# Optimization experiments

Measured on AMD Instinct MI355X. Metric: run time of the kernel, lower is better.

## Reference

```python
import jax, jax.numpy as jnp
import numpy as np

N = 100000   # nodes
E = 1600000  # edges (avg degree 16)
IN = 128     # in_size == out_size (required by layer stacking)
H = 4        # heads
D = 32       # per-head dim = out_size / heads
L = 3        # n_layers
NEG_SLOPE = 0.2  # DGL GATConv default leaky_relu slope


def setup_inputs() -> dict:
    key = jax.random.key(0)
    ks = jax.random.split(key, 7)
    h = jax.random.normal(ks[0], (N, IN), dtype=jnp.float32)
    src = jax.random.randint(ks[1], (E,), 0, N, dtype=jnp.int32)
    dst = jax.random.randint(ks[2], (E,), 0, N, dtype=jnp.int32)
    Ws = jax.random.normal(ks[3], (L, IN, H * D), dtype=jnp.float32) * 0.05
    attn_l = jax.random.normal(ks[4], (L, H, D), dtype=jnp.float32) * 0.05
    attn_r = jax.random.normal(ks[5], (L, H, D), dtype=jnp.float32) * 0.05
    bias = jnp.zeros((L, H, D), dtype=jnp.float32)
    return {"h": h, "src": src, "dst": dst, "Ws": Ws,
            "attn_l": attn_l, "attn_r": attn_r, "bias": bias}


def _gat_layer(h, src, dst, W, al, ar, b):
    # linear projection (no bias), reshape to heads
    ft = (h @ W).reshape(N, H, D)                       # [N,H,D]
    el = jnp.einsum('nhd,hd->nh', ft, al)               # [N,H]
    er = jnp.einsum('nhd,hd->nh', ft, ar)               # [N,H]
    # edge attention logits
    e = jax.nn.leaky_relu(el[src] + er[dst], NEG_SLOPE)  # [E,H]
    # segment softmax over incoming edges of each destination node
    m = jax.ops.segment_max(e, dst, num_segments=N)     # [N,H]
    m = jnp.where(jnp.isfinite(m), m, jnp.zeros_like(m))  # zero in-degree guard
    ee = jnp.exp(e - m[dst])                            # [E,H]
    den = jax.ops.segment_sum(ee, dst, num_segments=N)  # [N,H]
    a = ee / jnp.maximum(den[dst], 1e-9)                # [E,H]
    # weighted scatter-sum of source messages
    rst = jax.ops.segment_sum(ft[src] * a[:, :, None], dst, num_segments=N)  # [N,H,D]
    # residual (Identity: in_feats == H*D), bias, ELU activation
    rst = rst + h.reshape(N, H, D) + b
    return jax.nn.elu(rst), a


def reference(h, src, dst, Ws, attn_l, attn_r, bias):
    x = h
    a = None
    for i in range(L):
        out, a = _gat_layer(x, src, dst, Ws[i], attn_l[i], attn_r[i], bias[i])
        x = out.reshape(N, H * D)  # flatten(1)
    return x, a[:, :, None]  # ([N, H*D], [E, H, 1]) as DGL returns
```

## Files before the change

### kernel.cpp

```cpp
#include <hip/hip_runtime.h>
#include <hip/hip_bf16.h>
#include <math.h>

#define NN 100000
#define EE 1600000
#define IN_F 128
#define HH 4
#define DD 32
#define LL 3
#define NB_ 391
#define EPB 4096

typedef __bf16 bf16x8 __attribute__((ext_vector_type(8)));
typedef float f32x4 __attribute__((ext_vector_type(4)));

static __device__ __forceinline__ unsigned short f2bf(float x) {
    __hip_bfloat16 b = __float2bfloat16(x);
    return *reinterpret_cast<unsigned short*>(&b);
}

__global__ void wt_kernel(const float* __restrict__ Ws,
                          unsigned short* __restrict__ wt) {
    const int i = blockIdx.x * blockDim.x + threadIdx.x;
    if (i >= LL * IN_F * IN_F) return;
    const int l = i >> 14, r = i & 16383;
    const int n = r >> 7, k = r & 127;
    wt[i] = f2bf(Ws[(l << 14) + k * IN_F + n]);
}

template <bool F32A>
__global__ __launch_bounds__(256) void gemm_mfma_kernel(
    const void* __restrict__ a_src,
    const unsigned short* __restrict__ wt,
    const float* __restrict__ al,
    const float* __restrict__ ar,
    unsigned short* __restrict__ ft_bf,
    float* __restrict__ el,
    float* __restrict__ er) {
    const int wave = (blockIdx.x * blockDim.x + threadIdx.x) >> 6;
    const int lane = threadIdx.x & 63;
    const int base = wave * 16;
    if (base >= NN) return;
    const int c = lane & 15;
    const int quad = lane >> 4;

    const int arow = min(base + c, NN - 1);
    bf16x8 a[4];
    if (F32A) {
        const float4* xp = (const float4*)((const float*)a_src + (size_t)arow * IN_F);
#pragma unroll
        for (int kc = 0; kc < 4; ++kc) {
            const float4 lo = xp[(kc * 4 + quad) * 2];
            const float4 hi = xp[(kc * 4 + quad) * 2 + 1];
            union { unsigned short us[8]; bf16x8 v; } u;
            u.us[0] = f2bf(lo.x); u.us[1] = f2bf(lo.y);
            u.us[2] = f2bf(lo.z); u.us[3] = f2bf(lo.w);
            u.us[4] = f2bf(hi.x); u.us[5] = f2bf(hi.y);
            u.us[6] = f2bf(hi.z); u.us[7] = f2bf(hi.w);
            a[kc] = u.v;
        }
    } else {
        const bf16x8* ap = (const bf16x8*)((const unsigned short*)a_src + (size_t)arow * IN_F);
#pragma unroll
        for (int kc = 0; kc < 4; ++kc) a[kc] = ap[kc * 4 + quad];
    }

    f32x4 acc[8];
#pragma unroll
    for (int nt = 0; nt < 8; ++nt) {
        const bf16x8* bp = (const bf16x8*)(wt + (size_t)(nt * 16 + c) * IN_F);
        f32x4 d = {0.f, 0.f, 0.f, 0.f};
#pragma unroll
        for (int kc = 0; kc < 4; ++kc)
            d = __builtin_amdgcn_mfma_f32_16x16x32_bf16(a[kc], bp[kc * 4 + quad], d, 0, 0, 0);
        acc[nt] = d;
    }

#pragma unroll
    for (int r = 0; r < 4; ++r) {
        const int n = base + quad * 4 + r;
        if (n < NN) {
#pragma unroll
            for (int nt = 0; nt < 8; ++nt)
                ft_bf[(size_t)n * IN_F + nt * 16 + c] = f2bf(acc[nt][r]);
        }
    }

#pragma unroll
    for (int h = 0; h < 4; ++h) {
        float pl[4], pr[4];
#pragma unroll
        for (int r = 0; r < 4; ++r) {
            const float a0 = acc[2 * h][r], a1 = acc[2 * h + 1][r];
            pl[r] = a0 * al[h * 32 + c] + a1 * al[h * 32 + 16 + c];
            pr[r] = a0 * ar[h * 32 + c] + a1 * ar[h * 32 + 16 + c];
        }
#pragma unroll
        for (int off = 8; off >= 1; off >>= 1) {
#pragma unroll
            for (int r = 0; r < 4; ++r) {
                pl[r] += __shfl_xor(pl[r], off);
                pr[r] += __shfl_xor(pr[r], off);
            }
        }
        if (c == 0) {
#pragma unroll
            for (int r = 0; r < 4; ++r) {
                const int n = base + quad * 4 + r;
                if (n < NN) {
                    el[n * HH + h] = pl[r];
                    er[n * HH + h] = pr[r];
                }
            }
        }
    }
}


__global__ void bucket_hist_kernel(const int* __restrict__ dst,
                                   int* __restrict__ tot) {
    __shared__ int l[NB_];
    for (int b = threadIdx.x; b < NB_; b += 256) l[b] = 0;
    __syncthreads();
    const int e0 = blockIdx.x * EPB;
    const int e1 = min(e0 + EPB, EE);
    for (int e = e0 + threadIdx.x; e < e1; e += 256)
        atomicAdd(&l[dst[e] >> 8], 1);
    __syncthreads();
    for (int b = threadIdx.x; b < NB_; b += 256)
        if (l[b]) atomicAdd(&tot[b], l[b]);
}

__global__ void bucket_scan_kernel(const int* __restrict__ tot,
                                   int* __restrict__ base,
                                   int* __restrict__ cur) {
    __shared__ int tmp[512];
    const int tid = threadIdx.x;
    int v = (tid < NB_) ? tot[tid] : 0;
    tmp[tid] = v;
    __syncthreads();
    for (int off = 1; off < 512; off <<= 1) {
        int t = (tid >= off) ? tmp[tid - off] : 0;
        __syncthreads();
        if (tid >= off) tmp[tid] += t;
        __syncthreads();
    }
    if (tid < NB_) {
        const int excl = tmp[tid] - v;
        base[tid] = excl;
        cur[tid] = excl;
    }
    if (tid == 0) base[NB_] = EE;
}

__global__ void partition_kernel(const int* __restrict__ src,
                                 const int* __restrict__ dst,
                                 int* __restrict__ cur,
                                 int* __restrict__ bkt) {
    __shared__ int lcnt[NB_];
    __shared__ int lbase[NB_];
    const int tid = threadIdx.x;
    const int e0 = blockIdx.x * EPB;
    const int e1 = min(e0 + EPB, EE);
    for (int b = tid; b < NB_; b += 256) lcnt[b] = 0;
    __syncthreads();
    for (int e = e0 + tid; e < e1; e += 256)
        atomicAdd(&lcnt[dst[e] >> 8], 1);
    __syncthreads();
    for (int b = tid; b < NB_; b += 256) {
        const int c = lcnt[b];
        lbase[b] = c ? atomicAdd(&cur[b], c) : 0;
        lcnt[b] = 0;
    }
    __syncthreads();
    for (int e = e0 + tid; e < e1; e += 256) {
        const int d = dst[e];
        const int b = d >> 8;
        const int idx = atomicAdd(&lcnt[b], 1);
        bkt[lbase[b] + idx] = ((d & 255) << 17) | src[e];
    }
}

__global__ void bucket_sort_kernel(const int* __restrict__ bkt,
                                   const int* __restrict__ base,
                                   int* __restrict__ cnt,
                                   int* __restrict__ row_start,
                                   int* __restrict__ ssrc) {
    __shared__ int lcnt[256];
    __shared__ int loff[256];
    const int tid = threadIdx.x;
    const int b = blockIdx.x;
    const int s0 = base[b], s1 = base[b + 1];
    lcnt[tid] = 0;
    __syncthreads();
    for (int p = s0 + tid; p < s1; p += 256)
        atomicAdd(&lcnt[bkt[p] >> 17], 1);
    __syncthreads();
    const int v = lcnt[tid];
    loff[tid] = v;
    __syncthreads();
    for (int off = 1; off < 256; off <<= 1) {
        int t = (tid >= off) ? loff[tid - off] : 0;
        __syncthreads();
        if (tid >= off) loff[tid] += t;
        __syncthreads();
    }
    const int excl = loff[tid] - v;
    const int n = b * 256 + tid;
    if (n < NN) {
        cnt[n] = v;
        row_start[n] = s0 + excl;
    }
    __syncthreads();
    loff[tid] = excl;
    lcnt[tid] = 0;
    __syncthreads();
    for (int p = s0 + tid; p < s1; p += 256) {
        const int w = bkt[p];
        const int dl = w >> 17;
        const int idx = atomicAdd(&lcnt[dl], 1);
        ssrc[s0 + loff[dl] + idx] = w & 0x1FFFF;
    }
}

__global__ void aggregate_kernel(const uint4* __restrict__ ft4,
                                 const float* __restrict__ el,
                                 const float* __restrict__ er,
                                 const float* __restrict__ xin,
                                 const float* __restrict__ bias,
                                 const int* __restrict__ row_start,
                                 const int* __restrict__ cnt,
                                 const int* __restrict__ ssrc,
                                 float* __restrict__ out,
                                 unsigned short* __restrict__ out_bf,
                                 float* __restrict__ den_arr) {
    const int n = (blockIdx.x * blockDim.x + threadIdx.x) >> 6;
    const int lane = threadIdx.x & 63;
    if (n >= NN) return;
    const int e4 = lane >> 4;
    const int fq = lane & 15;
    const int h = fq >> 2;

    const float ern = er[n * HH + h];
    const int beg = row_start[n];
    const int end = beg + cnt[n];

    float acc[8] = {0.f, 0.f, 0.f, 0.f, 0.f, 0.f, 0.f, 0.f};
    float den = 0.f;

#define ACC8(E, W)                                                        \
    acc[0] = fmaf(E, __uint_as_float((W).x << 16), acc[0]);               \
    acc[1] = fmaf(E, __uint_as_float((W).x & 0xffff0000u), acc[1]);       \
    acc[2] = fmaf(E, __uint_as_float((W).y << 16), acc[2]);               \
    acc[3] = fmaf(E, __uint_as_float((W).y & 0xffff0000u), acc[3]);       \
    acc[4] = fmaf(E, __uint_as_float((W).z << 16), acc[4]);               \
    acc[5] = fmaf(E, __uint_as_float((W).z & 0xffff0000u), acc[5]);       \
    acc[6] = fmaf(E, __uint_as_float((W).w << 16), acc[6]);               \
    acc[7] = fmaf(E, __uint_as_float((W).w & 0xffff0000u), acc[7]);

    int p = beg;
    for (; p + 16 <= end; p += 16) {
        const int s0 = ssrc[p + e4];
        const int s1 = ssrc[p + 4 + e4];
        const int s2 = ssrc[p + 8 + e4];
        const int s3 = ssrc[p + 12 + e4];
        float ev0 = el[s0 * HH + h] + ern;
        float ev1 = el[s1 * HH + h] + ern;
        float ev2 = el[s2 * HH + h] + ern;
        float ev3 = el[s3 * HH + h] + ern;
        const uint4 w0 = ft4[(size_t)s0 * 16 + fq];
        const uint4 w1 = ft4[(size_t)s1 * 16 + fq];
        const uint4 w2 = ft4[(size_t)s2 * 16 + fq];
        const uint4 w3 = ft4[(size_t)s3 * 16 + fq];
        ev0 = ev0 > 0.f ? ev0 : 0.2f * ev0;
        ev1 = ev1 > 0.f ? ev1 : 0.2f * ev1;
        ev2 = ev2 > 0.f ? ev2 : 0.2f * ev2;
        ev3 = ev3 > 0.f ? ev3 : 0.2f * ev3;
        const float e0 = __expf(ev0);
        const float e1 = __expf(ev1);
        const float e2 = __expf(ev2);
        const float e3 = __expf(ev3);
        den += (e0 + e1) + (e2 + e3);
        ACC8(e0, w0)
        ACC8(e1, w1)
        ACC8(e2, w2)
        ACC8(e3, w3)
    }
    for (; p < end; p += 4) {
        const int pe = p + e4;
        const bool valid = pe < end;
        const int s = ssrc[valid ? pe : beg];
        float ev = el[s * HH + h] + ern;
        const uint4 w = ft4[(size_t)s * 16 + fq];
        ev = ev > 0.f ? ev : 0.2f * ev;
        const float e1 = valid ? __expf(ev) : 0.f;
        den += e1;
        ACC8(e1, w)
    }
#undef ACC8

#pragma unroll
    for (int off = 16; off < 64; off <<= 1) {
        den += __shfl_xor(den, off);
#pragma unroll
        for (int k = 0; k < 8; ++k) acc[k] += __shfl_xor(acc[k], off);
    }

    if (lane < 16) {
        if ((fq & 3) == 0) den_arr[n * HH + h] = den;
        const float inv = 1.f / fmaxf(den, 1e-9f);
        const float4 xi0 = ((const float4*)xin)[(size_t)n * 32 + fq * 2];
        const float4 xi1 = ((const float4*)xin)[(size_t)n * 32 + fq * 2 + 1];
        const float4 bb0 = ((const float4*)bias)[fq * 2];
        const float4 bb1 = ((const float4*)bias)[fq * 2 + 1];
        float v[8];
        v[0] = acc[0] * inv + xi0.x + bb0.x;
        v[1] = acc[1] * inv + xi0.y + bb0.y;
        v[2] = acc[2] * inv + xi0.z + bb0.z;
        v[3] = acc[3] * inv + xi0.w + bb0.w;
        v[4] = acc[4] * inv + xi1.x + bb1.x;
        v[5] = acc[5] * inv + xi1.y + bb1.y;
        v[6] = acc[6] * inv + xi1.z + bb1.z;
        v[7] = acc[7] * inv + xi1.w + bb1.w;
#pragma unroll
        for (int k = 0; k < 8; ++k)
            v[k] = v[k] > 0.f ? v[k] : __expf(v[k]) - 1.f;
        ((float4*)out)[(size_t)n * 32 + fq * 2] = make_float4(v[0], v[1], v[2], v[3]);
        ((float4*)out)[(size_t)n * 32 + fq * 2 + 1] = make_float4(v[4], v[5], v[6], v[7]);
        uint4 ob;
        ob.x = (unsigned int)f2bf(v[0]) | ((unsigned int)f2bf(v[1]) << 16);
        ob.y = (unsigned int)f2bf(v[2]) | ((unsigned int)f2bf(v[3]) << 16);
        ob.z = (unsigned int)f2bf(v[4]) | ((unsigned int)f2bf(v[5]) << 16);
        ob.w = (unsigned int)f2bf(v[6]) | ((unsigned int)f2bf(v[7]) << 16);
        ((uint4*)out_bf)[(size_t)n * 16 + fq] = ob;
    }
}

__global__ void attn_out_kernel(const int* __restrict__ src,
                                const int* __restrict__ dst,
                                const float* __restrict__ el,
                                const float* __restrict__ er,
                                const float* __restrict__ den,
                                float* __restrict__ a_out) {
    const int e = blockIdx.x * blockDim.x + threadIdx.x;
    if (e >= EE) return;
    const int s = src[e], d = dst[e];
    const float4 l4 = ((const float4*)el)[s];
    const float4 r4 = ((const float4*)er)[d];
    const float4 dn = ((const float4*)den)[d];
    float v[4] = {l4.x + r4.x, l4.y + r4.y, l4.z + r4.z, l4.w + r4.w};
    float dv[4] = {dn.x, dn.y, dn.z, dn.w};
    float4 o;
    float* op = &o.x;
#pragma unroll
    for (int hh = 0; hh < 4; ++hh) {
        float t = v[hh] > 0.f ? v[hh] : 0.2f * v[hh];
        op[hh] = __expf(t) / fmaxf(dv[hh], 1e-9f);
    }
    ((float4*)a_out)[e] = o;
}

extern "C" void kernel_launch(void* const* d_in, const int* in_sizes, int n_in,
                              void* d_out, int out_size, void* d_ws, size_t ws_size,
                              hipStream_t stream) {
    const float* h    = (const float*)d_in[0];
    const int*   src  = (const int*)  d_in[1];
    const int*   dst  = (const int*)  d_in[2];
    const float* Ws   = (const float*)d_in[3];
    const float* al   = (const float*)d_in[4];
    const float* ar   = (const float*)d_in[5];
    const float* bias = (const float*)d_in[6];

    float* out_x = (float*)d_out;
    float* out_a = out_x + (size_t)NN * IN_F;
    unsigned short* x_bf = (unsigned short*)out_a;

    char* ws = (char*)d_ws;
    unsigned short* ft_bf = (unsigned short*)ws;
    float* bufA = (float*)(ft_bf + (size_t)NN * IN_F);
    float* el   = bufA + (size_t)NN * IN_F;
    float* er   = el + (size_t)NN * HH;
    float* den  = er + (size_t)NN * HH;
    int*   cnt        = (int*)(den + (size_t)NN * HH);
    int*   row_start  = cnt + NN;
    int*   bucket_tot = row_start + NN;
    int*   bucket_base= bucket_tot + 512;
    int*   bucket_cur = bucket_base + 512;
    int*   ssrc       = bucket_cur + 512;
    unsigned short* wt = (unsigned short*)(ssrc + EE);
    int* bkt = (int*)bufA;

    wt_kernel<<<(LL * IN_F * IN_F + 255) / 256, 256, 0, stream>>>(Ws, wt);

    hipMemsetAsync(bucket_tot, 0, 512 * sizeof(int), stream);
    const int ebks = (EE + EPB - 1) / EPB;
    bucket_hist_kernel<<<ebks, 256, 0, stream>>>(dst, bucket_tot);
    bucket_scan_kernel<<<1, 512, 0, stream>>>(bucket_tot, bucket_base, bucket_cur);
    partition_kernel<<<ebks, 256, 0, stream>>>(src, dst, bucket_cur, bkt);
    bucket_sort_kernel<<<NB_, 256, 0, stream>>>(bkt, bucket_base, cnt, row_start, ssrc);

    const float* xin[LL]  = {h, bufA, out_x};
    float*       xout[LL] = {bufA, out_x, out_x};
    const int gemm_blocks = ((NN + 15) / 16 + 3) / 4;

    for (int i = 0; i < LL; ++i) {
        const float* all_ = al + (size_t)i * HH * DD;
        const float* arl = ar + (size_t)i * HH * DD;
        const float* bl  = bias + (size_t)i * HH * DD;

        if (i == 0) {
            gemm_mfma_kernel<true><<<gemm_blocks, 256, 0, stream>>>(
                (const void*)h, wt + (size_t)i * IN_F * IN_F, all_, arl, ft_bf, el, er);
        } else {
            gemm_mfma_kernel<false><<<gemm_blocks, 256, 0, stream>>>(
                (const void*)x_bf, wt + (size_t)i * IN_F * IN_F, all_, arl, ft_bf, el, er);
        }
        aggregate_kernel<<<(NN + 3) / 4, 256, 0, stream>>>(
            (const uint4*)ft_bf, el, er, xin[i], bl, row_start, cnt, ssrc,
            xout[i], x_bf, den);
    }
    attn_out_kernel<<<(EE + 255) / 256, 256, 0, stream>>>(src, dst, el, er, den, out_a);
}
```

Measured before the change: 583.2 us.

## Stage GEMM output through LDS, interleave er/den, add nontemporal streaming accesses

The GEMM kernel now writes its bf16 tile into LDS and then stores full 16-byte row segments to global memory. Before, each lane scattered 2-byte stores. er and den are interleaved into one array so the attention-output kernel fetches both with adjacent loads. Nontemporal loads and stores are applied to streaming data (edge indices, residual input, outputs) to reduce cache pollution. The cost is extra LDS use and a block barrier in the GEMM kernel, which may reduce occupancy.

```diff
diff --git a/kernel.cpp b/kernel.cpp
--- a/kernel.cpp
+++ b/kernel.cpp
@@ -13,6 +13,7 @@
 
 typedef __bf16 bf16x8 __attribute__((ext_vector_type(8)));
 typedef float f32x4 __attribute__((ext_vector_type(4)));
+typedef unsigned int u32x4 __attribute__((ext_vector_type(4)));
 
 static __device__ __forceinline__ unsigned short f2bf(float x) {
     __hip_bfloat16 b = __float2bfloat16(x);
@@ -36,80 +37,93 @@
     const float* __restrict__ ar,
     unsigned short* __restrict__ ft_bf,
     float* __restrict__ el,
-    float* __restrict__ er) {
+    float* __restrict__ erden) {
+    __shared__ unsigned short lds_t[4 * 16 * 136];
     const int wave = (blockIdx.x * blockDim.x + threadIdx.x) >> 6;
+    const int w = (threadIdx.x >> 6) & 3;
     const int lane = threadIdx.x & 63;
     const int base = wave * 16;
-    if (base >= NN) return;
+    const bool active = base < NN;
     const int c = lane & 15;
     const int quad = lane >> 4;
 
-    const int arow = min(base + c, NN - 1);
-    bf16x8 a[4];
-    if (F32A) {
-        const float4* xp = (const float4*)((const float*)a_src + (size_t)arow * IN_F);
-#pragma unroll
-        for (int kc = 0; kc < 4; ++kc) {
-            const float4 lo = xp[(kc * 4 + quad) * 2];
-            const float4 hi = xp[(kc * 4 + quad) * 2 + 1];
-            union { unsigned short us[8]; bf16x8 v; } u;
-            u.us[0] = f2bf(lo.x); u.us[1] = f2bf(lo.y);
-            u.us[2] = f2bf(lo.z); u.us[3] = f2bf(lo.w);
-            u.us[4] = f2bf(hi.x); u.us[5] = f2bf(hi.y);
-            u.us[6] = f2bf(hi.z); u.us[7] = f2bf(hi.w);
-            a[kc] = u.v;
+    f32x4 acc[8];
+    if (active) {
+        const int arow = min(base + c, NN - 1);
+        bf16x8 a[4];
+        if (F32A) {
+            const float4* xp = (const float4*)((const float*)a_src + (size_t)arow * IN_F);
+#pragma unroll
+            for (int kc = 0; kc < 4; ++kc) {
+                const float4 lo = xp[(kc * 4 + quad) * 2];
+                const float4 hi = xp[(kc * 4 + quad) * 2 + 1];
+                union { unsigned short us[8]; bf16x8 v; } u;
+                u.us[0] = f2bf(lo.x); u.us[1] = f2bf(lo.y);
+                u.us[2] = f2bf(lo.z); u.us[3] = f2bf(lo.w);
+                u.us[4] = f2bf(hi.x); u.us[5] = f2bf(hi.y);
+                u.us[6] = f2bf(hi.z); u.us[7] = f2bf(hi.w);
+                a[kc] = u.v;
+            }
+        } else {
+            const bf16x8* ap = (const bf16x8*)((const unsigned short*)a_src + (size_t)arow * IN_F);
+#pragma unroll
+            for (int kc = 0; kc < 4; ++kc) a[kc] = ap[kc * 4 + quad];
         }
-    } else {
-        const bf16x8* ap = (const bf16x8*)((const unsigned short*)a_src + (size_t)arow * IN_F);
-#pragma unroll
-        for (int kc = 0; kc < 4; ++kc) a[kc] = ap[kc * 4 + quad];
-    }
-
-    f32x4 acc[8];
-#pragma unroll
-    for (int nt = 0; nt < 8; ++nt) {
-        const bf16x8* bp = (const bf16x8*)(wt + (size_t)(nt * 16 + c) * IN_F);
-        f32x4 d = {0.f, 0.f, 0.f, 0.f};
-#pragma unroll
-        for (int kc = 0; kc < 4; ++kc)
-            d = __builtin_amdgcn_mfma_f32_16x16x32_bf16(a[kc], bp[kc * 4 + quad], d, 0, 0, 0);
-        acc[nt] = d;
-    }
-
-#pragma unroll
-    for (int r = 0; r < 4; ++r) {
-        const int n = base + quad * 4 + r;
-        if (n < NN) {
-#pragma unroll
-            for (int nt = 0; nt < 8; ++nt)
-                ft_bf[(size_t)n * IN_F + nt * 16 + c] = f2bf(acc[nt][r]);
+
+#pragma unroll
+        for (int nt = 0; nt < 8; ++nt) {
+            const bf16x8* bp = (const bf16x8*)(wt + (size_t)(nt * 16 + c) * IN_F);
+            f32x4 d = {0.f, 0.f, 0.f, 0.f};
+#pragma unroll
+            for (int kc = 0; kc < 4; ++kc)
+                d = __builtin_amdgcn_mfma_f32_16x16x32_bf16(a[kc], bp[kc * 4 + quad], d, 0, 0, 0);
+            acc[nt] = d;
         }
-    }
-
-#pragma unroll
-    for (int h = 0; h < 4; ++h) {
-        float pl[4], pr[4];
-#pragma unroll
-        for (int r = 0; r < 4; ++r) {
-            const float a0 = acc[2 * h][r], a1 = acc[2 * h + 1][r];
-            pl[r] = a0 * al[h * 32 + c] + a1 * al[h * 32 + 16 + c];
-            pr[r] = a0 * ar[h * 32 + c] + a1 * ar[h * 32 + 16 + c];
+
+#pragma unroll
+        for (int nt = 0; nt < 8; ++nt)
+#pragma unroll
+            for (int r = 0; r < 4; ++r)
+                lds_t[w * 2176 + (quad * 4 + r) * 136 + nt * 16 + c] = f2bf(acc[nt][r]);
+    }
+    __syncthreads();
+    if (active) {
+        const int row = lane >> 2;
+        const int seg = lane & 3;
+        const int n_row = base + row;
+        if (n_row < NN) {
+            const unsigned short* lp = &lds_t[w * 2176 + row * 136 + seg * 8];
+            uint4* gp = (uint4*)(ft_bf + (size_t)n_row * IN_F) + seg;
+#pragma unroll
+            for (int it = 0; it < 4; ++it)
+                gp[it * 4] = *(const uint4*)(lp + it * 32);
         }
-#pragma unroll
-        for (int off = 8; off >= 1; off >>= 1) {
+
+#pragma unroll
+        for (int h = 0; h < 4; ++h) {
+            float pl[4], pr[4];
 #pragma unroll
             for (int r = 0; r < 4; ++r) {
-                pl[r] += __shfl_xor(pl[r], off);
-                pr[r] += __shfl_xor(pr[r], off);
+                const float a0 = acc[2 * h][r], a1 = acc[2 * h + 1][r];
+                pl[r] = a0 * al[h * 32 + c] + a1 * al[h * 32 + 16 + c];
+                pr[r] = a0 * ar[h * 32 + c] + a1 * ar[h * 32 + 16 + c];
             }
-        }
-        if (c == 0) {
-#pragma unroll
-            for (int r = 0; r < 4; ++r) {
-                const int n = base + quad * 4 + r;
-                if (n < NN) {
-                    el[n * HH + h] = pl[r];
-                    er[n * HH + h] = pr[r];
+#pragma unroll
+            for (int off = 8; off >= 1; off >>= 1) {
+#pragma unroll
+                for (int r = 0; r < 4; ++r) {
+                    pl[r] += __shfl_xor(pl[r], off);
+                    pr[r] += __shfl_xor(pr[r], off);
+                }
+            }
+            if (c == 0) {
+#pragma unroll
+                for (int r = 0; r < 4; ++r) {
+                    const int n = base + quad * 4 + r;
+                    if (n < NN) {
+                        el[n * HH + h] = pl[r];
+                        erden[(size_t)n * 8 + h] = pr[r];
+                    }
                 }
             }
         }
@@ -225,15 +239,14 @@
 
 __global__ void aggregate_kernel(const uint4* __restrict__ ft4,
                                  const float* __restrict__ el,
-                                 const float* __restrict__ er,
+                                 float* __restrict__ erden,
                                  const float* __restrict__ xin,
                                  const float* __restrict__ bias,
                                  const int* __restrict__ row_start,
                                  const int* __restrict__ cnt,
                                  const int* __restrict__ ssrc,
                                  float* __restrict__ out,
-                                 unsigned short* __restrict__ out_bf,
-                                 float* __restrict__ den_arr) {
+                                 unsigned short* __restrict__ out_bf) {
     const int n = (blockIdx.x * blockDim.x + threadIdx.x) >> 6;
     const int lane = threadIdx.x & 63;
     if (n >= NN) return;
@@ -241,7 +254,7 @@
     const int fq = lane & 15;
     const int h = fq >> 2;
 
-    const float ern = er[n * HH + h];
+    const float ern = erden[(size_t)n * 8 + h];
     const int beg = row_start[n];
     const int end = beg + cnt[n];
 
@@ -260,10 +273,10 @@
 
     int p = beg;
     for (; p + 16 <= end; p += 16) {
-        const int s0 = ssrc[p + e4];
-        const int s1 = ssrc[p + 4 + e4];
-        const int s2 = ssrc[p + 8 + e4];
-        const int s3 = ssrc[p + 12 + e4];
+        const int s0 = __builtin_nontemporal_load(&ssrc[p + e4]);
+        const int s1 = __builtin_nontemporal_load(&ssrc[p + 4 + e4]);
+        const int s2 = __builtin_nontemporal_load(&ssrc[p + 8 + e4]);
+        const int s3 = __builtin_nontemporal_load(&ssrc[p + 12 + e4]);
         float ev0 = el[s0 * HH + h] + ern;
         float ev1 = el[s1 * HH + h] + ern;
         float ev2 = el[s2 * HH + h] + ern;
@@ -289,7 +302,7 @@
     for (; p < end; p += 4) {
         const int pe = p + e4;
         const bool valid = pe < end;
-        const int s = ssrc[valid ? pe : beg];
+        const int s = __builtin_nontemporal_load(&ssrc[valid ? pe : beg]);
         float ev = el[s * HH + h] + ern;
         const uint4 w = ft4[(size_t)s * 16 + fq];
         ev = ev > 0.f ? ev : 0.2f * ev;
@@ -307,10 +320,10 @@
     }
 
     if (lane < 16) {
-        if ((fq & 3) == 0) den_arr[n * HH + h] = den;
+        if ((fq & 3) == 0) erden[(size_t)n * 8 + 4 + h] = den;
         const float inv = 1.f / fmaxf(den, 1e-9f);
-        const float4 xi0 = ((const float4*)xin)[(size_t)n * 32 + fq * 2];
-        const float4 xi1 = ((const float4*)xin)[(size_t)n * 32 + fq * 2 + 1];
+        const f32x4 xi0 = __builtin_nontemporal_load((const f32x4*)xin + (size_t)n * 32 + fq * 2);
+        const f32x4 xi1 = __builtin_nontemporal_load((const f32x4*)xin + (size_t)n * 32 + fq * 2 + 1);
         const float4 bb0 = ((const float4*)bias)[fq * 2];
         const float4 bb1 = ((const float4*)bias)[fq * 2 + 1];
         float v[8];
@@ -325,39 +338,40 @@
 #pragma unroll
         for (int k = 0; k < 8; ++k)
             v[k] = v[k] > 0.f ? v[k] : __expf(v[k]) - 1.f;
-        ((float4*)out)[(size_t)n * 32 + fq * 2] = make_float4(v[0], v[1], v[2], v[3]);
-        ((float4*)out)[(size_t)n * 32 + fq * 2 + 1] = make_float4(v[4], v[5], v[6], v[7]);
-        uint4 ob;
+        f32x4 o0 = {v[0], v[1], v[2], v[3]};
+        f32x4 o1 = {v[4], v[5], v[6], v[7]};
+        __builtin_nontemporal_store(o0, (f32x4*)out + (size_t)n * 32 + fq * 2);
+        __builtin_nontemporal_store(o1, (f32x4*)out + (size_t)n * 32 + fq * 2 + 1);
+        u32x4 ob;
         ob.x = (unsigned int)f2bf(v[0]) | ((unsigned int)f2bf(v[1]) << 16);
         ob.y = (unsigned int)f2bf(v[2]) | ((unsigned int)f2bf(v[3]) << 16);
         ob.z = (unsigned int)f2bf(v[4]) | ((unsigned int)f2bf(v[5]) << 16);
         ob.w = (unsigned int)f2bf(v[6]) | ((unsigned int)f2bf(v[7]) << 16);
-        ((uint4*)out_bf)[(size_t)n * 16 + fq] = ob;
+        __builtin_nontemporal_store(ob, (u32x4*)out_bf + (size_t)n * 16 + fq);
     }
 }
 
 __global__ void attn_out_kernel(const int* __restrict__ src,
                                 const int* __restrict__ dst,
                                 const float* __restrict__ el,
-                                const float* __restrict__ er,
-                                const float* __restrict__ den,
+                                const float* __restrict__ erden,
                                 float* __restrict__ a_out) {
     const int e = blockIdx.x * blockDim.x + threadIdx.x;
     if (e >= EE) return;
-    const int s = src[e], d = dst[e];
+    const int s = __builtin_nontemporal_load(&src[e]);
+    const int d = __builtin_nontemporal_load(&dst[e]);
     const float4 l4 = ((const float4*)el)[s];
-    const float4 r4 = ((const float4*)er)[d];
-    const float4 dn = ((const float4*)den)[d];
+    const float4 r4 = *(const float4*)(erden + (size_t)d * 8);
+    const float4 dn = *(const float4*)(erden + (size_t)d * 8 + 4);
     float v[4] = {l4.x + r4.x, l4.y + r4.y, l4.z + r4.z, l4.w + r4.w};
     float dv[4] = {dn.x, dn.y, dn.z, dn.w};
-    float4 o;
-    float* op = &o.x;
+    f32x4 o;
 #pragma unroll
     for (int hh = 0; hh < 4; ++hh) {
         float t = v[hh] > 0.f ? v[hh] : 0.2f * v[hh];
-        op[hh] = __expf(t) / fmaxf(dv[hh], 1e-9f);
-    }
-    ((float4*)a_out)[e] = o;
+        o[hh] = __expf(t) / fmaxf(dv[hh], 1e-9f);
+    }
+    __builtin_nontemporal_store(o, (f32x4*)a_out + e);
 }
 
 extern "C" void kernel_launch(void* const* d_in, const int* in_sizes, int n_in,
@@ -379,9 +393,8 @@
     unsigned short* ft_bf = (unsigned short*)ws;
     float* bufA = (float*)(ft_bf + (size_t)NN * IN_F);
     float* el   = bufA + (size_t)NN * IN_F;
-    float* er   = el + (size_t)NN * HH;
-    float* den  = er + (size_t)NN * HH;
-    int*   cnt        = (int*)(den + (size_t)NN * HH);
+    float* erden= el + (size_t)NN * HH;
+    int*   cnt        = (int*)(erden + (size_t)NN * 8);
     int*   row_start  = cnt + NN;
     int*   bucket_tot = row_start + NN;
     int*   bucket_base= bucket_tot + 512;
@@ -410,14 +423,14 @@
 
         if (i == 0) {
             gemm_mfma_kernel<true><<<gemm_blocks, 256, 0, stream>>>(
-                (const void*)h, wt + (size_t)i * IN_F * IN_F, all_, arl, ft_bf, el, er);
+                (const void*)h, wt + (size_t)i * IN_F * IN_F, all_, arl, ft_bf, el, erden);
         } else {
             gemm_mfma_kernel<false><<<gemm_blocks, 256, 0, stream>>>(
-                (const void*)x_bf, wt + (size_t)i * IN_F * IN_F, all_, arl, ft_bf, el, er);
+                (const void*)x_bf, wt + (size_t)i * IN_F * IN_F, all_, arl, ft_bf, el, erden);
         }
         aggregate_kernel<<<(NN + 3) / 4, 256, 0, stream>>>(
-            (const uint4*)ft_bf, el, er, xin[i], bl, row_start, cnt, ssrc,
-            xout[i], x_bf, den);
-    }
-    attn_out_kernel<<<(EE + 255) / 256, 256, 0, stream>>>(src, dst, el, er, den, out_a);
-}
+            (const uint4*)ft_bf, el, erden, xin[i], bl, row_start, cnt, ssrc,
+            xout[i], x_bf);
+    }
+    attn_out_kernel<<<(EE + 255) / 256, 256, 0, stream>>>(src, dst, el, erden, out_a);
+}
```

After: 609.6 us. 4.5% more time.
